# Kernel optimization log

Measured on AMD Instinct MI355X. Metric: run time of the kernel, lower is better.

Reference implementation:

```python
import jax, jax.numpy as jnp
import numpy as np

B, D, NH, HH, WW = 16, 384, 12, 48, 48
MLP = 4 * D


def _dwconv(x_blc, w, b, H, W):
    # depthwise 3x3 conv on (B,L,C) token map laid out as HxW
    Bsz, L, C = x_blc.shape
    xn = x_blc.reshape(Bsz, H, W, C).transpose(0, 3, 1, 2)  # NCHW
    y = jax.lax.conv_general_dilated(
        xn, w, (1, 1), 'SAME', feature_group_count=C,
        dimension_numbers=('NCHW', 'OIHW', 'NCHW'))
    y = y + b[None, :, None, None]
    return y.transpose(0, 2, 3, 1).reshape(Bsz, L, C)


def _ln(x, w, b):
    m = jnp.mean(x, -1, keepdims=True)
    v = jnp.mean(jnp.square(x - m), -1, keepdims=True)
    return (x - m) * jax.lax.rsqrt(v + 1e-5) * w + b


def _rope_tables(H, W, C):
    k_max = C // 4  # feature_dim // (2 * len((h, w)))
    theta = 1.0 / (10000.0 ** (jnp.arange(k_max, dtype=jnp.float32) / k_max))
    ah = jnp.broadcast_to((jnp.arange(H, dtype=jnp.float32)[:, None] * theta)[:, None, :], (H, W, k_max))
    aw = jnp.broadcast_to((jnp.arange(W, dtype=jnp.float32)[:, None] * theta)[None, :, :], (H, W, k_max))
    ang = jnp.concatenate([ah, aw], -1)  # (H, W, C//2)
    return jnp.cos(ang), jnp.sin(ang)


def _rope(x, cos, sin):
    # x: (B,H,W,C); complex rotation on consecutive pairs of the last dim
    xr = x.reshape(*x.shape[:-1], -1, 2)
    a, b2 = xr[..., 0], xr[..., 1]
    out = jnp.stack([cos * a - sin * b2, sin * a + cos * b2], -1)
    return out.reshape(x.shape)


def _forward(x, H, W, cpe1_w, cpe1_b, norm1_w, norm1_b, in_proj_w, in_proj_b,
             act_proj_w, act_proj_b, dwc_w, dwc_b, qk_w, qk_b, lepe_w, lepe_b,
             out_proj_w, out_proj_b, cpe2_w, cpe2_b, norm2_w, norm2_b,
             fc1_w, fc1_b, fc2_w, fc2_b):
    Bsz, L, C = x.shape
    nh = NH
    hd = C // nh

    x = x + _dwconv(x, cpe1_w, cpe1_b, H, W)
    shortcut = x
    xn = _ln(x, norm1_w, norm1_b)
    act_res = jax.nn.silu(xn @ act_proj_w.T + act_proj_b)
    xi = xn @ in_proj_w.T + in_proj_b
    xi = jax.nn.silu(_dwconv(xi, dwc_w, dwc_b, H, W))

    # --- linear (kernelized) attention with RoPE ---
    qk = xi @ qk_w.T + qk_b  # (B, L, 2C)
    q = jax.nn.elu(qk[..., :C]) + 1.0
    k = jax.nn.elu(qk[..., C:]) + 1.0
    cos, sin = _rope_tables(H, W, C)
    q_rope = _rope(q.reshape(Bsz, H, W, C), cos, sin).reshape(Bsz, L, nh, hd).transpose(0, 2, 1, 3)
    k_rope = _rope(k.reshape(Bsz, H, W, C), cos, sin).reshape(Bsz, L, nh, hd).transpose(0, 2, 1, 3)
    qh = q.reshape(Bsz, L, nh, hd).transpose(0, 2, 1, 3)
    kh = k.reshape(Bsz, L, nh, hd).transpose(0, 2, 1, 3)
    vh = xi.reshape(Bsz, L, nh, hd).transpose(0, 2, 1, 3)

    z = 1.0 / (jnp.einsum('bhnd,bhd->bhn', qh, kh.mean(axis=2)) + 1e-6)  # (B,nh,L)
    kv = jnp.einsum('bhnd,bhne->bhde', k_rope, vh) / L                   # (B,nh,hd,hd)
    att = jnp.einsum('bhnd,bhde->bhne', q_rope, kv) * z[..., None]
    att = att.transpose(0, 2, 1, 3).reshape(Bsz, L, C)
    att = att + _dwconv(xi, lepe_w, lepe_b, H, W)  # lepe on v (== xi)

    out = (att * act_res) @ out_proj_w.T + out_proj_b
    x = shortcut + out
    x = x + _dwconv(x, cpe2_w, cpe2_b, H, W)
    xn2 = _ln(x, norm2_w, norm2_b)
    h1 = jax.nn.gelu(xn2 @ fc1_w.T + fc1_b, approximate=False)
    x = x + (h1 @ fc2_w.T + fc2_b)
    return x


def setup_inputs() -> dict:
    key = jax.random.key(0)
    ks = jax.random.split(key, 16)
    def w(k, shape, s=0.02):
        return jax.random.normal(k, shape, jnp.float32) * s
    return {
        'x': jax.random.normal(ks[0], (B, HH * WW, D), jnp.float32),
        'H': HH, 'W': WW,
        'cpe1_w': w(ks[1], (D, 1, 3, 3)), 'cpe1_b': jnp.zeros((D,), jnp.float32),
        'norm1_w': jnp.ones((D,), jnp.float32), 'norm1_b': jnp.zeros((D,), jnp.float32),
        'in_proj_w': w(ks[2], (D, D)), 'in_proj_b': jnp.zeros((D,), jnp.float32),
        'act_proj_w': w(ks[3], (D, D)), 'act_proj_b': jnp.zeros((D,), jnp.float32),
        'dwc_w': w(ks[4], (D, 1, 3, 3)), 'dwc_b': jnp.zeros((D,), jnp.float32),
        'qk_w': w(ks[5], (2 * D, D)), 'qk_b': jnp.zeros((2 * D,), jnp.float32),
        'lepe_w': w(ks[6], (D, 1, 3, 3)), 'lepe_b': jnp.zeros((D,), jnp.float32),
        'out_proj_w': w(ks[7], (D, D)), 'out_proj_b': jnp.zeros((D,), jnp.float32),
        'cpe2_w': w(ks[8], (D, 1, 3, 3)), 'cpe2_b': jnp.zeros((D,), jnp.float32),
        'norm2_w': jnp.ones((D,), jnp.float32), 'norm2_b': jnp.zeros((D,), jnp.float32),
        'fc1_w': w(ks[9], (MLP, D)), 'fc1_b': jnp.zeros((MLP,), jnp.float32),
        'fc2_w': w(ks[10], (D, MLP)), 'fc2_b': jnp.zeros((D,), jnp.float32),
    }


def reference(x, H, W, cpe1_w, cpe1_b, norm1_w, norm1_b, in_proj_w, in_proj_b,
              act_proj_w, act_proj_b, dwc_w, dwc_b, qk_w, qk_b, lepe_w, lepe_b,
              out_proj_w, out_proj_b, cpe2_w, cpe2_b, norm2_w, norm2_b,
              fc1_w, fc1_b, fc2_w, fc2_b):
    return _forward(x, H, W, cpe1_w, cpe1_b, norm1_w, norm1_b, in_proj_w, in_proj_b,
                    act_proj_w, act_proj_b, dwc_w, dwc_b, qk_w, qk_b, lepe_w, lepe_b,
                    out_proj_w, out_proj_b, cpe2_w, cpe2_b, norm2_w, norm2_b,
                    fc1_w, fc1_b, fc2_w, fc2_b)
```

## Files before the change

kernel.cpp:

```cpp
#include <hip/hip_runtime.h>
#include <hip/hip_bf16.h>
#include <math.h>


#define L_TOK 2304
#define DIM   384
#define NHEADS 12
#define BATCH 16
#define HIMG  48
#define WIMG  48
#define UNITB ((size_t)L_TOK * DIM)

typedef unsigned short u16;
typedef __attribute__((ext_vector_type(8))) short bf16x8;
typedef __attribute__((ext_vector_type(8))) unsigned short u16x8;
typedef __attribute__((ext_vector_type(4))) float f32x4;

enum { M_BIAS = 0, M_SILU = 1, M_ELU1 = 2, M_GELU = 3, M_RES = 4 };

__device__ __forceinline__ float frcp(float x) { return __builtin_amdgcn_rcpf(x); }
__device__ __forceinline__ float siluf(float x) { return x * frcp(1.0f + __expf(-x)); }
__device__ __forceinline__ float geluf(float x) {
    float t = x * fmaf(x * x, 0.0713548162726f, 1.59576912161f);
    return x * frcp(1.0f + __expf(-t));
}
__device__ __forceinline__ u16 f2bf(float f) {
    union { __hip_bfloat16 h; u16 u; } c;
    c.h = __float2bfloat16(f);
    return c.u;
}
__device__ __forceinline__ float bf2f(u16 u) { return __uint_as_float(((unsigned)u) << 16); }
__device__ __forceinline__ float4 bf2f4(ushort4 v) {
    return (float4){bf2f(v.x), bf2f(v.y), bf2f(v.z), bf2f(v.w)};
}
__device__ __forceinline__ void vmwait(int n) {
    if (n == 0)       asm volatile("s_waitcnt vmcnt(0)" ::: "memory");
    else if (n == 4)  asm volatile("s_waitcnt vmcnt(4)" ::: "memory");
    else if (n == 8)  asm volatile("s_waitcnt vmcnt(8)" ::: "memory");
    else if (n == 12) asm volatile("s_waitcnt vmcnt(12)" ::: "memory");
    else              asm volatile("s_waitcnt vmcnt(0)" ::: "memory");
}

__global__ void sentinel_k(float* out, float v) { out[0] = v; }

__global__ __launch_bounds__(256) void cvtw_k(const float* __restrict__ src, u16* __restrict__ dst) {
    int i = blockIdx.x * 256 + threadIdx.x;
    float4 v = ((const float4*)src)[i];
    ushort4 o;
    o.x = f2bf(v.x); o.y = f2bf(v.y); o.z = f2bf(v.z); o.w = f2bf(v.w);
    ((ushort4*)dst)[i] = o;
}

__global__ __launch_bounds__(256) void rope_tab_k(float* __restrict__ cosT, float* __restrict__ sinT) {
    int i = blockIdx.x * 256 + threadIdx.x;
    if (i >= L_TOK * 192) return;
    int n = i / 192, p = i % 192;
    int h = n / WIMG, w = n % WIMG;
    int j = (p < 96) ? p : p - 96;
    float pos = (p < 96) ? (float)h : (float)w;
    float theta = expf(-(float)j * (9.210340371976184f / 96.0f));
    float ang = pos * theta;
    cosT[i] = cosf(ang);
    sinT[i] = sinf(ang);
}

#define FMA4(s, a, ww) { s.x = fmaf(a.x, ww.x, s.x); s.y = fmaf(a.y, ww.y, s.y); \
                         s.z = fmaf(a.z, ww.z, s.z); s.w = fmaf(a.w, ww.w, s.w); }

__device__ __forceinline__ void dw_remap(int& vbx, int& vby) {
    const int nstr = gridDim.y;
    vbx = blockIdx.x; vby = blockIdx.y;
    if ((nstr & 7) == 0 || (nstr & 7) == 4) {
        if ((nstr & 7) == 0) {
            const int lin = blockIdx.x + blockIdx.y * gridDim.x;
            const int x = lin & 7, k = lin >> 3;
            vby = x * (nstr >> 3) + k / gridDim.x;
            vbx = k - (k / gridDim.x) * gridDim.x;
        }
    }
}

__global__ __launch_bounds__(256) void dwconvf_k(const float* __restrict__ src,
                                                 const float* __restrict__ wgt,
                                                 const float* __restrict__ bias,
                                                 float* __restrict__ outf) {
    int vbx, vby;
    dw_remap(vbx, vby);
    const int col = vbx * 256 + threadIdx.x;
    const int strip = vby & 3;
    const int b = vby >> 2;
    const int cg = col % 96, w = col / 96;
    const int rs = WIMG * DIM;
    const size_t ibase = (size_t)b * UNITB + (size_t)w * DIM + cg * 4;
    const float* srcb = src + ibase;
    const float4 z4 = {0.f, 0.f, 0.f, 0.f};
    float4 w9[9];
#pragma unroll
    for (int t = 0; t < 9; ++t) {
        const int c = cg * 4;
        w9[t] = (float4){wgt[(c + 0) * 9 + t], wgt[(c + 1) * 9 + t],
                         wgt[(c + 2) * 9 + t], wgt[(c + 3) * 9 + t]};
    }
    const float4 bv = ((const float4*)bias)[cg];
    float4 A0, A1, A2, B0, B1, B2, C0, C1, C2;
    auto ldrow = [&](int hh, float4& L0, float4& L1, float4& L2) {
        if ((unsigned)hh >= (unsigned)HIMG) { L0 = z4; L1 = z4; L2 = z4; return; }
        const float* p = srcb + (size_t)hh * rs;
        L0 = (w > 0)        ? *(const float4*)(p - DIM) : z4;
        L1 = *(const float4*)p;
        L2 = (w < WIMG - 1) ? *(const float4*)(p + DIM) : z4;
    };
    const int h0 = strip * 12;
    ldrow(h0 - 1, A0, A1, A2);
    ldrow(h0,     B0, B1, B2);
    for (int h = h0; h < h0 + 12; ++h) {
        ldrow(h + 1, C0, C1, C2);
        float4 s = bv;
        FMA4(s, A0, w9[0]); FMA4(s, A1, w9[1]); FMA4(s, A2, w9[2]);
        FMA4(s, B0, w9[3]); FMA4(s, B1, w9[4]); FMA4(s, B2, w9[5]);
        FMA4(s, C0, w9[6]); FMA4(s, C1, w9[7]); FMA4(s, C2, w9[8]);
        const size_t idx = ibase + (size_t)h * rs;
        s.x += B1.x; s.y += B1.y; s.z += B1.z; s.w += B1.w;
        *(float4*)(outf + idx) = s;
        A0 = B0; A1 = B1; A2 = B2;
        B0 = C0; B1 = C1; B2 = C2;
    }
}

__global__ __launch_bounds__(256) void dwconvb_k(const u16* __restrict__ src,
                                                 const float* __restrict__ wgt,
                                                 const float* __restrict__ bias,
                                                 const u16* __restrict__ att,
                                                 const u16* __restrict__ act,
                                                 u16* __restrict__ outb, int mode) {
    int vbx, vby;
    dw_remap(vbx, vby);
    const int col = vbx * 256 + threadIdx.x;
    const int strip = vby & 3;
    const int b = vby >> 2;
    const int cg = col % 96, w = col / 96;
    const int rs = WIMG * DIM;
    const size_t ibase = (size_t)b * UNITB + (size_t)w * DIM + cg * 4;
    const u16* srcb = src + ibase;
    const float4 z4 = {0.f, 0.f, 0.f, 0.f};
    float4 w9[9];
#pragma unroll
    for (int t = 0; t < 9; ++t) {
        const int c = cg * 4;
        w9[t] = (float4){wgt[(c + 0) * 9 + t], wgt[(c + 1) * 9 + t],
                         wgt[(c + 2) * 9 + t], wgt[(c + 3) * 9 + t]};
    }
    const float4 bv = ((const float4*)bias)[cg];
    float4 A0, A1, A2, B0, B1, B2, C0, C1, C2;
    auto ldrow = [&](int hh, float4& L0, float4& L1, float4& L2) {
        if ((unsigned)hh >= (unsigned)HIMG) { L0 = z4; L1 = z4; L2 = z4; return; }
        const u16* p = srcb + (size_t)hh * rs;
        L0 = (w > 0)        ? bf2f4(*(const ushort4*)(p - DIM)) : z4;
        L1 = bf2f4(*(const ushort4*)p);
        L2 = (w < WIMG - 1) ? bf2f4(*(const ushort4*)(p + DIM)) : z4;
    };
    const int h0 = strip * 12;
    ldrow(h0 - 1, A0, A1, A2);
    ldrow(h0,     B0, B1, B2);
    for (int h = h0; h < h0 + 12; ++h) {
        ldrow(h + 1, C0, C1, C2);
        float4 s = bv;
        FMA4(s, A0, w9[0]); FMA4(s, A1, w9[1]); FMA4(s, A2, w9[2]);
        FMA4(s, B0, w9[3]); FMA4(s, B1, w9[4]); FMA4(s, B2, w9[5]);
        FMA4(s, C0, w9[6]); FMA4(s, C1, w9[7]); FMA4(s, C2, w9[8]);
        const size_t idx = ibase + (size_t)h * rs;
        ushort4 ob;
        if (mode == 1) {
            ob = (ushort4){f2bf(siluf(s.x)), f2bf(siluf(s.y)), f2bf(siluf(s.z)), f2bf(siluf(s.w))};
        } else {
            float4 a4 = bf2f4(*(const ushort4*)(att + idx));
            float4 m4 = bf2f4(*(const ushort4*)(act + idx));
            ob = (ushort4){f2bf((a4.x + s.x) * m4.x), f2bf((a4.y + s.y) * m4.y),
                           f2bf((a4.z + s.z) * m4.z), f2bf((a4.w + s.w) * m4.w)};
        }
        *(ushort4*)(outb + idx) = ob;
        A0 = B0; A1 = B1; A2 = B2;
        B0 = C0; B1 = C1; B2 = C2;
    }
}

__global__ __launch_bounds__(256) void ln_k(const float* __restrict__ in,
                                            const float* __restrict__ w,
                                            const float* __restrict__ b,
                                            u16* __restrict__ out) {
    const int dd = blockIdx.x;
    const int vb = (dd & 7) * (gridDim.x >> 3) + (dd >> 3);
    const int row = vb * 4 + (threadIdx.x >> 6);
    const int lane = threadIdx.x & 63;
    const float* x = in + (size_t)row * DIM;
    float v[6];
    float s = 0.f;
#pragma unroll
    for (int i = 0; i < 6; ++i) { v[i] = x[lane + i * 64]; s += v[i]; }
#pragma unroll
    for (int o = 32; o > 0; o >>= 1) s += __shfl_xor(s, o, 64);
    const float mean = s * (1.0f / DIM);
    float q = 0.f;
#pragma unroll
    for (int i = 0; i < 6; ++i) { float d = v[i] - mean; q = fmaf(d, d, q); }
#pragma unroll
    for (int o = 32; o > 0; o >>= 1) q += __shfl_xor(q, o, 64);
    const float rs = 1.0f / sqrtf(q * (1.0f / DIM) + 1e-5f);
    u16* o2 = out + (size_t)row * DIM;
#pragma unroll
    for (int i = 0; i < 6; ++i) {
        int d = lane + i * 64;
        o2[d] = f2bf(fmaf((v[i] - mean) * rs, w[d], b[d]));
    }
}

#define CHK 64
template<int K>
__global__ __launch_bounds__(256, 4) void gemm_sk(const u16* __restrict__ A, int lda,
                                                  const u16* __restrict__ Wt, int ldw,
                                                  const float* __restrict__ bias,
                                                  const float* __restrict__ bias2,
                                                  const float* __restrict__ res,
                                                  float* __restrict__ Cf, u16* __restrict__ Cb,
                                                  u16* __restrict__ Cb2,
                                                  int ldc, int mode, int mode2) {
    constexpr int NT = K / 32;
    constexpr int NCH = K / CHK;
    __shared__ u16 smem[16384];
    u16* const Bbuf[2] = {smem, smem + 8192};
    const int tid = threadIdx.x;
    const int l = tid & 63;
    const int w = tid >> 6;
    const int fr = l & 15, kb = l >> 4;
    const int T = gridDim.x * gridDim.y;
    const int d = blockIdx.y * gridDim.x + blockIdx.x;
    int flat = d;
    if ((T & 7) == 0) { const int q8 = T >> 3; flat = (d & 7) * q8 + (d >> 3); }
    const int n0 = (flat % gridDim.x) * 128;
    const int m0 = (flat / gridDim.x) * 128;
    const int sw = (fr & 7) << 4;

    f32x4 acc[2][8];
#pragma unroll
    for (int i = 0; i < 2; ++i)
#pragma unroll
        for (int j = 0; j < 8; ++j) acc[i][j] = (f32x4){0.f, 0.f, 0.f, 0.f};

    const u16* Ar0 = A + (size_t)(m0 + w * 32 + fr) * lda + kb * 8;
    const u16* Ar1 = Ar0 + (size_t)16 * lda;

    auto STAGE = [&](u16* buf, int cc) {
        const int ck0 = cc * CHK;
#pragma unroll
        for (int q = 0; q < 4; ++q) {
            const int c16 = q * 256 + tid;
            const int col = c16 >> 3;
            const int kb16 = c16 & 7;
            const int koff = ((kb16 * 16) ^ ((col & 7) << 4)) >> 1;
            const u16* g = Wt + (size_t)(n0 + col) * ldw + ck0 + koff;
            __builtin_amdgcn_global_load_lds(
                (const __attribute__((address_space(1))) void*)g,
                (__attribute__((address_space(3))) void*)(buf + (size_t)(q * 256 + w * 64) * 8),
                16, 0, 0);
        }
    };

    bf16x8 pA[4][2];
    STAGE(Bbuf[0], 0);
    __builtin_amdgcn_sched_barrier(0);
#pragma unroll
    for (int i = 0; i < 4; ++i) {
        pA[i][0] = *(const bf16x8*)(Ar0 + i * 32);
        pA[i][1] = *(const bf16x8*)(Ar1 + i * 32);
    }
    __builtin_amdgcn_sched_barrier(0);
    STAGE(Bbuf[1], 1);
    __builtin_amdgcn_sched_barrier(0);
    vmwait(12);
    __builtin_amdgcn_s_barrier();

#pragma unroll
    for (int c = 0; c < NCH; ++c) {
        const u16* bp = Bbuf[c & 1];
#pragma unroll
        for (int ks = 0; ks < 2; ++ks) {
            const int t = 2 * c + ks;
            bf16x8 a0 = pA[t & 3][0], a1 = pA[t & 3][1];
            if (t + 4 < NT) {
                pA[t & 3][0] = *(const bf16x8*)(Ar0 + (t + 4) * 32);
                pA[t & 3][1] = *(const bf16x8*)(Ar1 + (t + 4) * 32);
            }
            const int kpart = (ks * 64 + kb * 16) ^ sw;
            const char* bsb = (const char*)bp + fr * 128 + kpart;
#pragma unroll
            for (int ni = 0; ni < 8; ++ni) {
                bf16x8 bfrag = *(const bf16x8*)(bsb + ni * (16 * 128));
                acc[0][ni] = __builtin_amdgcn_mfma_f32_16x16x32_bf16(a0, bfrag, acc[0][ni], 0, 0, 0);
                acc[1][ni] = __builtin_amdgcn_mfma_f32_16x16x32_bf16(a1, bfrag, acc[1][ni], 0, 0, 0);
            }
        }
        __builtin_amdgcn_sched_barrier(0);
        __builtin_amdgcn_s_barrier();
        __builtin_amdgcn_sched_barrier(0);
        if (c + 2 < NCH) STAGE(Bbuf[c & 1], c + 2);
        __builtin_amdgcn_sched_barrier(0);
        if (c + 1 < NCH)
            vmwait((c < NCH - 2) ? 8 : 0);
    }

    const int orow = (l >> 4) * 4, ocol = l & 15;
    if (Cb != nullptr) {
        const bool is2 = (Cb2 != nullptr) && (n0 >= DIM);
        u16* dst = is2 ? Cb2 : Cb;
        const int ldcs = is2 ? DIM : ldc;
        const int nc0 = is2 ? (n0 - DIM) : n0;
        const float* bp2 = is2 ? bias2 : bias;
        const int md = is2 ? mode2 : mode;
#pragma unroll
        for (int mi = 0; mi < 2; ++mi)
#pragma unroll
            for (int ni = 0; ni < 8; ++ni) {
                const int colL = ni * 16 + ocol;
                const float bv = bp2[nc0 + colL];
#pragma unroll
                for (int r = 0; r < 4; ++r) {
                    const int rowL = w * 32 + mi * 16 + orow + r;
                    float v = acc[mi][ni][r] + bv;
                    if (md == M_SILU)      v = siluf(v);
                    else if (md == M_ELU1) v = (v > 0.f) ? (v + 1.f) : __expf(v);
                    else if (md == M_GELU) v = geluf(v);
                    smem[rowL * 128 + (colL ^ ((rowL & 7) << 3))] = f2bf(v);
                }
            }
        __builtin_amdgcn_s_barrier();
        const int rr = tid >> 4, cc = tid & 15;
#pragma unroll
        for (int it = 0; it < 8; ++it) {
            const int row = it * 16 + rr;
            u16x8 v = *(const u16x8*)&smem[row * 128 + ((cc * 8) ^ ((row & 7) << 3))];
            *(u16x8*)(dst + (size_t)(m0 + row) * ldcs + nc0 + cc * 8) = v;
        }
    } else {
        float* smf = (float*)smem;
#pragma unroll
        for (int p = 0; p < 2; ++p) {
            if (p) __builtin_amdgcn_s_barrier();
#pragma unroll
            for (int mi = 0; mi < 2; ++mi)
#pragma unroll
                for (int ni = 0; ni < 4; ++ni) {
                    const int colL = ni * 16 + ocol;
                    const float bv = bias[n0 + p * 64 + colL];
#pragma unroll
                    for (int r = 0; r < 4; ++r) {
                        const int rowL = w * 32 + mi * 16 + orow + r;
                        float v = acc[mi][p * 4 + ni][r] + bv;
                        if (mode == M_SILU)      v = siluf(v);
                        else if (mode == M_ELU1) v = (v > 0.f) ? (v + 1.f) : __expf(v);
                        else if (mode == M_GELU) v = geluf(v);
                        smf[rowL * 64 + (colL ^ ((rowL & 3) << 4))] = v;
                    }
                }
            __builtin_amdgcn_s_barrier();
            const int rr = tid >> 4, cc = tid & 15;
#pragma unroll
            for (int it = 0; it < 8; ++it) {
                const int row = it * 16 + rr;
                float4 v = *(const float4*)&smf[row * 64 + ((cc * 4) ^ ((row & 3) << 4))];
                const size_t oi = (size_t)(m0 + row) * ldc + n0 + p * 64 + cc * 4;
                if (res) {
                    float4 rv = *(const float4*)(res + oi);
                    v.x += rv.x; v.y += rv.y; v.z += rv.z; v.w += rv.w;
                }
                *(float4*)(Cf + oi) = v;
            }
        }
    }
}

__global__ __launch_bounds__(384) void kmean_part_k(const u16* __restrict__ kbuf, float* __restrict__ part, int nb) {
    const int b = blockIdx.x, chunk = blockIdx.y;
    const int c = threadIdx.x;
    const u16* p = kbuf + ((size_t)(b * L_TOK + chunk * 256)) * DIM + c;
    float s = 0.f;
    for (int n = 0; n < 256; ++n) s += bf2f(p[(size_t)n * DIM]);
    part[(size_t)(chunk * nb + b) * DIM + c] = s;
}

__global__ __launch_bounds__(384) void kmean_fin_k(const float* __restrict__ part, float* __restrict__ km, int nb) {
    const int b = blockIdx.x, c = threadIdx.x;
    float s = 0.f;
#pragma unroll
    for (int ch = 0; ch < 9; ++ch) s += part[(size_t)(ch * nb + b) * DIM + c];
    km[b * DIM + c] = s * (1.0f / L_TOK);
}

__global__ __launch_bounds__(256) void z_k(const u16* __restrict__ q, const float* __restrict__ km,
                                           float* __restrict__ z) {
    const int dd = blockIdx.x;
    const int vb = (dd & 7) * (gridDim.x >> 3) + (dd >> 3);
    const int row = vb * 4 + (threadIdx.x >> 6);
    const int lane = threadIdx.x & 63;
    const int b = row / L_TOK;
    const u16* qr = q + (size_t)row * DIM;
    const float* kb = km + b * DIM;
    float s = 0.f;
#pragma unroll
    for (int i = 0; i < 6; ++i) { int c = lane + i * 64; s += bf2f(qr[c]) * kb[c]; }
#pragma unroll
    for (int o = 32; o > 0; o >>= 1) s += __shfl_xor(s, o, 64);
    if (lane == 0) z[row] = 1.0f / (s + 1e-6f);
}

__global__ __launch_bounds__(256) void kv_part_k(const u16* __restrict__ kbuf, const u16* __restrict__ xi,
                                                 const float* __restrict__ cosT, const float* __restrict__ sinT,
                                                 float* __restrict__ part) {
    const int bh = blockIdx.x >> 2, chunk = blockIdx.x & 3;
    const int b = bh / NHEADS, h = bh % NHEADS;
    __shared__ float ks[64][33];
    __shared__ float vs[64][33];
    const int tid = threadIdx.x;
    const int e0 = (tid & 15) * 2;
    const int d0 = (tid >> 4) * 2;
    float acc00 = 0.f, acc01 = 0.f, acc10 = 0.f, acc11 = 0.f;
    const int nbeg = chunk * 576, nend = nbeg + 576;
    for (int n0 = nbeg; n0 < nend; n0 += 64) {
#pragma unroll
        for (int j = 0; j < 4; ++j) {
            int pi = tid + j * 256;
            int tn = pi >> 4;
            int pd = pi & 15;
            int n = n0 + tn;
            unsigned kk = *(const unsigned*)(kbuf + ((size_t)(b * L_TOK + n)) * DIM + h * 32 + pd * 2);
            float ka = bf2f((u16)(kk & 0xffffu)), kb2 = bf2f((u16)(kk >> 16));
            float cs = cosT[n * 192 + h * 16 + pd];
            float sn = sinT[n * 192 + h * 16 + pd];
            ks[tn][pd * 2]     = cs * ka - sn * kb2;
            ks[tn][pd * 2 + 1] = sn * ka + cs * kb2;
        }
#pragma unroll
        for (int j = 0; j < 4; ++j) {
            int pi = tid + j * 256;
            int tn = pi >> 4;
            int dd = (pi & 15) * 2;
            unsigned vv = *(const unsigned*)(xi + ((size_t)(b * L_TOK + n0 + tn)) * DIM + h * 32 + dd);
            vs[tn][dd]     = bf2f((u16)(vv & 0xffffu));
            vs[tn][dd + 1] = bf2f((u16)(vv >> 16));
        }
        __syncthreads();
#pragma unroll 8
        for (int n = 0; n < 64; ++n) {
            float k0v = ks[n][d0], k1v = ks[n][d0 + 1];
            float v0 = vs[n][e0], v1 = vs[n][e0 + 1];
            acc00 = fmaf(k0v, v0, acc00);
            acc01 = fmaf(k0v, v1, acc01);
            acc10 = fmaf(k1v, v0, acc10);
            acc11 = fmaf(k1v, v1, acc11);
        }
        __syncthreads();
    }
    float* o = part + ((size_t)blockIdx.x * 32 + d0) * 32 + e0;
    o[0] = acc00; o[1] = acc01;
    o[32] = acc10; o[33] = acc11;
}

__global__ __launch_bounds__(256) void kv_fin_k(const float* __restrict__ part, u16* __restrict__ kvt) {
    const int bh = blockIdx.x;
    const int tid = threadIdx.x;
#pragma unroll
    for (int i = tid; i < 1024; i += 256) {
        const int e = i >> 5, dd = i & 31;
        float s = 0.f;
#pragma unroll
        for (int c = 0; c < 4; ++c) s += part[((size_t)(bh * 4 + c)) * 1024 + dd * 32 + e];
        kvt[(size_t)bh * 1024 + i] = f2bf(s * (1.0f / L_TOK));
    }
}

__global__ __launch_bounds__(256) void attm_k(const u16* __restrict__ q, const u16* __restrict__ kvt,
                                              const float* __restrict__ z,
                                              const float* __restrict__ cosT, const float* __restrict__ sinT,
                                              u16* __restrict__ out) {
    __shared__ u16 ost[128 * 32];
    const int tid = threadIdx.x, l = tid & 63, w = tid >> 6;
    const int b = blockIdx.y / NHEADS, h = blockIdx.y % NHEADS;
    const int m0 = blockIdx.x * 128;
    const int fr = l & 15, kb = l >> 4;

    f32x4 acc[2][2];
#pragma unroll
    for (int i = 0; i < 2; ++i)
#pragma unroll
        for (int j = 0; j < 2; ++j) acc[i][j] = (f32x4){0.f, 0.f, 0.f, 0.f};

    const int p0 = h * 16 + kb * 4;
    bf16x8 afr[2];
#pragma unroll
    for (int mi = 0; mi < 2; ++mi) {
        const int n = m0 + w * 32 + mi * 16 + fr;
        bf16x8 raw = *(const bf16x8*)(q + ((size_t)(b * L_TOK + n)) * DIM + h * 32 + kb * 8);
        float4 cs = *(const float4*)(cosT + (size_t)n * 192 + p0);
        float4 sn = *(const float4*)(sinT + (size_t)n * 192 + p0);
        union { u16 u[8]; bf16x8 v; } pk;
        float a0, a1;
        a0 = bf2f((u16)raw[0]); a1 = bf2f((u16)raw[1]);
        pk.u[0] = f2bf(cs.x * a0 - sn.x * a1); pk.u[1] = f2bf(sn.x * a0 + cs.x * a1);
        a0 = bf2f((u16)raw[2]); a1 = bf2f((u16)raw[3]);
        pk.u[2] = f2bf(cs.y * a0 - sn.y * a1); pk.u[3] = f2bf(sn.y * a0 + cs.y * a1);
        a0 = bf2f((u16)raw[4]); a1 = bf2f((u16)raw[5]);
        pk.u[4] = f2bf(cs.z * a0 - sn.z * a1); pk.u[5] = f2bf(sn.z * a0 + cs.z * a1);
        a0 = bf2f((u16)raw[6]); a1 = bf2f((u16)raw[7]);
        pk.u[6] = f2bf(cs.w * a0 - sn.w * a1); pk.u[7] = f2bf(sn.w * a0 + cs.w * a1);
        afr[mi] = pk.v;
    }
    bf16x8 bfr[2];
    const u16* kvh = kvt + (size_t)(b * NHEADS + h) * 1024;
#pragma unroll
    for (int ni = 0; ni < 2; ++ni)
        bfr[ni] = *(const bf16x8*)(kvh + (ni * 16 + fr) * 32 + kb * 8);
#pragma unroll
    for (int mi = 0; mi < 2; ++mi)
#pragma unroll
        for (int ni = 0; ni < 2; ++ni)
            acc[mi][ni] = __builtin_amdgcn_mfma_f32_16x16x32_bf16(afr[mi], bfr[ni], acc[mi][ni], 0, 0, 0);

    const int orow = (l >> 4) * 4, ocol = l & 15;
#pragma unroll
    for (int mi = 0; mi < 2; ++mi) {
        float zz[4];
#pragma unroll
        for (int r = 0; r < 4; ++r)
            zz[r] = z[b * L_TOK + m0 + w * 32 + mi * 16 + orow + r];
#pragma unroll
        for (int ni = 0; ni < 2; ++ni) {
#pragma unroll
            for (int r = 0; r < 4; ++r) {
                const int rowL = w * 32 + mi * 16 + orow + r;
                ost[rowL * 32 + ni * 16 + ocol] = f2bf(acc[mi][ni][r] * zz[r]);
            }
        }
    }
    __syncthreads();
#pragma unroll
    for (int it = 0; it < 2; ++it) {
        const int ch = it * 256 + tid;
        const int row = ch >> 2, c8 = (ch & 3) * 8;
        u16x8 v = *(const u16x8*)&ost[row * 32 + c8];
        *(u16x8*)(out + ((size_t)(b * L_TOK + m0 + row)) * DIM + h * 32 + c8) = v;
    }
}

extern "C" void kernel_launch(void* const* d_in, const int* in_sizes, int n_in,
                              void* d_out, int out_size, void* d_ws, size_t ws_size,
                              hipStream_t stream) {
    const float* x       = (const float*)d_in[0];
    const float* cpe1_w  = (const float*)d_in[3];
    const float* cpe1_b  = (const float*)d_in[4];
    const float* norm1_w = (const float*)d_in[5];
    const float* norm1_b = (const float*)d_in[6];
    const float* in_w    = (const float*)d_in[7];
    const float* in_b    = (const float*)d_in[8];
    const float* act_w   = (const float*)d_in[9];
    const float* act_b   = (const float*)d_in[10];
    const float* dwc_w   = (const float*)d_in[11];
    const float* dwc_b   = (const float*)d_in[12];
    const float* qk_w    = (const float*)d_in[13];
    const float* qk_b    = (const float*)d_in[14];
    const float* lepe_w  = (const float*)d_in[15];
    const float* lepe_b  = (const float*)d_in[16];
    const float* outp_w  = (const float*)d_in[17];
    const float* outp_b  = (const float*)d_in[18];
    const float* cpe2_w  = (const float*)d_in[19];
    const float* cpe2_b  = (const float*)d_in[20];
    const float* norm2_w = (const float*)d_in[21];
    const float* norm2_b = (const float*)d_in[22];
    const float* fc1_w   = (const float*)d_in[23];
    const float* fc1_b   = (const float*)d_in[24];
    const float* fc2_w   = (const float*)d_in[25];
    const float* fc2_b   = (const float*)d_in[26];
    float* out = (float*)d_out;

    float* ws = (float*)d_ws;
    const size_t TAB = (size_t)L_TOK * 192;
    const size_t NW_IN = 147456, NW_QK = 294912, NW_FC = 589824;
    const size_t WBF_U16 = NW_IN * 3 + NW_QK + NW_FC * 2;
    const size_t KVP = 4 * (size_t)BATCH * NHEADS * 1024;
    const size_t ZB  = (size_t)BATCH * L_TOK;
    const size_t SMALL = 2 * TAB + (size_t)BATCH * DIM + 9 * (size_t)BATCH * DIM
                       + (size_t)BATCH * NHEADS * 1024 + KVP + ZB + WBF_U16 / 2;
    float* cosT = ws;
    float* sinT = cosT + TAB;
    float* km   = sinT + TAB;
    float* part = km + (size_t)BATCH * DIM;
    float* kvb  = part + 9 * (size_t)BATCH * DIM;
    float* kvp  = kvb + (size_t)BATCH * NHEADS * 1024;
    float* zb   = kvp + KVP;
    u16*   kvt  = (u16*)kvb;
    u16*   wb_in  = (u16*)(zb + ZB);
    u16*   wb_act = wb_in + NW_IN;
    u16*   wb_qk  = wb_act + NW_IN;
    u16*   wb_out = wb_qk + NW_QK;
    u16*   wb_fc1 = wb_out + NW_IN;
    u16*   wb_fc2 = wb_fc1 + NW_FC;
    float* gbuf = ws + SMALL;

    const size_t avail = (ws_size / 4 > SMALL) ? (ws_size / 4 - SMALL) : 0;
    int nb = 0;
    for (int cand = BATCH; cand >= 1; cand >>= 1)
        if (9 * (size_t)cand * UNITB / 2 <= avail) { nb = cand; break; }
    if (nb == 0) {
        sentinel_k<<<1, 1, 0, stream>>>(out, (float)(ws_size >> 20));
        return;
    }

    cvtw_k<<<(int)(NW_IN / 1024), 256, 0, stream>>>(in_w, wb_in);
    cvtw_k<<<(int)(NW_IN / 1024), 256, 0, stream>>>(act_w, wb_act);
    cvtw_k<<<(int)(NW_QK / 1024), 256, 0, stream>>>(qk_w, wb_qk);
    cvtw_k<<<(int)(NW_IN / 1024), 256, 0, stream>>>(outp_w, wb_out);
    cvtw_k<<<(int)(NW_FC / 1024), 256, 0, stream>>>(fc1_w, wb_fc1);
    cvtw_k<<<(int)(NW_FC / 1024), 256, 0, stream>>>(fc2_w, wb_fc2);
    rope_tab_k<<<(int)((TAB + 255) / 256), 256, 0, stream>>>(cosT, sinT);

    for (int b0 = 0; b0 < BATCH; b0 += nb) {
        const size_t goff = (size_t)b0 * UNITB;
        const size_t GU   = (size_t)nb * UNITB;
        float* W0 = gbuf;
        float* W1 = gbuf + GU;
        float* W2 = gbuf + 2 * GU;
        u16*   Wb = (u16*)(gbuf + 4 * GU);
        float* O  = out + goff;
        const float* Xg = x + goff;
        u16* xi0p = (u16*)W2;
        u16* actp = (u16*)W2 + GU;

        const dim3 DWG(18, nb * 4);
        const dim3 G384(3, nb * 18), G768(6, nb * 18), G1536(12, nb * 18);

        dwconvf_k<<<DWG, 256, 0, stream>>>(Xg, cpe1_w, cpe1_b, W0);
        ln_k<<<nb * 576, 256, 0, stream>>>(W0, norm1_w, norm1_b, (u16*)W1);
        gemm_sk<384><<<G768, 256, 0, stream>>>((u16*)W1, DIM, wb_in, DIM, in_b, act_b, nullptr,
                                               nullptr, xi0p, actp, DIM, M_BIAS, M_SILU);
        dwconvb_k<<<DWG, 256, 0, stream>>>(xi0p, dwc_w, dwc_b, nullptr, nullptr, Wb, 1);
        gemm_sk<384><<<G768, 256, 0, stream>>>(Wb, DIM, wb_qk, DIM, qk_b, qk_b + DIM, nullptr,
                                               nullptr, (u16*)W1, (u16*)O, DIM, M_ELU1, M_ELU1);
        kmean_part_k<<<dim3(nb, 9), 384, 0, stream>>>((u16*)O, part, nb);
        kmean_fin_k<<<nb, 384, 0, stream>>>(part, km, nb);
        z_k<<<nb * 576, 256, 0, stream>>>((u16*)W1, km, zb);
        kv_part_k<<<nb * NHEADS * 4, 256, 0, stream>>>((u16*)O, Wb, cosT, sinT, kvp);
        kv_fin_k<<<nb * NHEADS, 256, 0, stream>>>(kvp, kvt);
        attm_k<<<dim3(18, nb * NHEADS), 256, 0, stream>>>((u16*)W1, kvt, zb, cosT, sinT, (u16*)O);
        dwconvb_k<<<DWG, 256, 0, stream>>>(Wb, lepe_w, lepe_b, (const u16*)O, actp,
                                           (u16*)W1, 3);
        gemm_sk<384><<<G384, 256, 0, stream>>>((u16*)W1, DIM, wb_out, DIM, outp_b, nullptr, W0,
                                               W2, nullptr, nullptr, DIM, M_RES, M_RES);
        dwconvf_k<<<DWG, 256, 0, stream>>>(W2, cpe2_w, cpe2_b, W0);
        ln_k<<<nb * 576, 256, 0, stream>>>(W0, norm2_w, norm2_b, (u16*)W1);
        gemm_sk<384><<<G1536, 256, 0, stream>>>((u16*)W1, DIM, wb_fc1, DIM, fc1_b, nullptr, nullptr,
                                                nullptr, (u16*)W2, nullptr, 1536, M_GELU, M_GELU);
        gemm_sk<1536><<<G384, 256, 0, stream>>>((u16*)W2, 1536, wb_fc2, 1536, fc2_b, nullptr, W0,
                                                O, nullptr, nullptr, DIM, M_RES, M_RES);
    }
}
```

Baseline: 510.5 us.

## Fuse depthwise CPE conv with LayerNorm into a single kernel

Replaces the separate fp32 depthwise-conv kernel and LayerNorm kernel with one kernel, dwln_k. Each 384-thread block handles 4 tokens, computes the 3x3 conv plus residual directly from neighbours, writes the fp32 result, and then reduces mean and variance through shared memory to emit the normalized bf16 output. This removes one launch and the re-read of the fp32 conv output by the LN pass. In exchange, the row-streaming register reuse of conv inputs is lost, so neighbouring rows are re-read from cache. Variance is now computed as E[x^2]-mean^2, which is less numerically robust.

```diff
diff --git a/kernel.cpp b/kernel.cpp
--- a/kernel.cpp
+++ b/kernel.cpp
@@ -67,33 +67,23 @@
 #define FMA4(s, a, ww) { s.x = fmaf(a.x, ww.x, s.x); s.y = fmaf(a.y, ww.y, s.y); \
                          s.z = fmaf(a.z, ww.z, s.z); s.w = fmaf(a.w, ww.w, s.w); }
 
-__device__ __forceinline__ void dw_remap(int& vbx, int& vby) {
-    const int nstr = gridDim.y;
-    vbx = blockIdx.x; vby = blockIdx.y;
-    if ((nstr & 7) == 0 || (nstr & 7) == 4) {
-        if ((nstr & 7) == 0) {
-            const int lin = blockIdx.x + blockIdx.y * gridDim.x;
-            const int x = lin & 7, k = lin >> 3;
-            vby = x * (nstr >> 3) + k / gridDim.x;
-            vbx = k - (k / gridDim.x) * gridDim.x;
-        }
-    }
-}
-
-__global__ __launch_bounds__(256) void dwconvf_k(const float* __restrict__ src,
-                                                 const float* __restrict__ wgt,
-                                                 const float* __restrict__ bias,
-                                                 float* __restrict__ outf) {
-    int vbx, vby;
-    dw_remap(vbx, vby);
-    const int col = vbx * 256 + threadIdx.x;
-    const int strip = vby & 3;
-    const int b = vby >> 2;
-    const int cg = col % 96, w = col / 96;
-    const int rs = WIMG * DIM;
-    const size_t ibase = (size_t)b * UNITB + (size_t)w * DIM + cg * 4;
-    const float* srcb = src + ibase;
-    const float4 z4 = {0.f, 0.f, 0.f, 0.f};
+__global__ __launch_bounds__(384) void dwln_k(const float* __restrict__ src,
+                                              const float* __restrict__ wgt,
+                                              const float* __restrict__ bias,
+                                              const float* __restrict__ nw,
+                                              const float* __restrict__ nb_,
+                                              float* __restrict__ outf,
+                                              u16* __restrict__ outn) {
+    const int T = 12 * gridDim.y;
+    int lin = blockIdx.x + blockIdx.y * 12;
+    { const int x = lin & 7, k = lin >> 3; lin = x * (T >> 3) + k; }
+    const int vbx = lin % 12, vby = lin / 12;
+    const int tok = threadIdx.x / 96, cg = threadIdx.x % 96;
+    const int w = vbx * 4 + tok;
+    const int h = vby % HIMG;
+    const int b = vby / HIMG;
+    const size_t base = (size_t)b * UNITB + cg * 4;
+
     float4 w9[9];
 #pragma unroll
     for (int t = 0; t < 9; ++t) {
@@ -101,29 +91,62 @@
         w9[t] = (float4){wgt[(c + 0) * 9 + t], wgt[(c + 1) * 9 + t],
                          wgt[(c + 2) * 9 + t], wgt[(c + 3) * 9 + t]};
     }
-    const float4 bv = ((const float4*)bias)[cg];
-    float4 A0, A1, A2, B0, B1, B2, C0, C1, C2;
-    auto ldrow = [&](int hh, float4& L0, float4& L1, float4& L2) {
-        if ((unsigned)hh >= (unsigned)HIMG) { L0 = z4; L1 = z4; L2 = z4; return; }
-        const float* p = srcb + (size_t)hh * rs;
-        L0 = (w > 0)        ? *(const float4*)(p - DIM) : z4;
-        L1 = *(const float4*)p;
-        L2 = (w < WIMG - 1) ? *(const float4*)(p + DIM) : z4;
-    };
-    const int h0 = strip * 12;
-    ldrow(h0 - 1, A0, A1, A2);
-    ldrow(h0,     B0, B1, B2);
-    for (int h = h0; h < h0 + 12; ++h) {
-        ldrow(h + 1, C0, C1, C2);
-        float4 s = bv;
-        FMA4(s, A0, w9[0]); FMA4(s, A1, w9[1]); FMA4(s, A2, w9[2]);
-        FMA4(s, B0, w9[3]); FMA4(s, B1, w9[4]); FMA4(s, B2, w9[5]);
-        FMA4(s, C0, w9[6]); FMA4(s, C1, w9[7]); FMA4(s, C2, w9[8]);
-        const size_t idx = ibase + (size_t)h * rs;
-        s.x += B1.x; s.y += B1.y; s.z += B1.z; s.w += B1.w;
-        *(float4*)(outf + idx) = s;
-        A0 = B0; A1 = B1; A2 = B2;
-        B0 = C0; B1 = C1; B2 = C2;
+    float4 s = ((const float4*)bias)[cg];
+    float4 ctr = {0.f, 0.f, 0.f, 0.f};
+#pragma unroll
+    for (int dh = 0; dh < 3; ++dh) {
+        const int hh = h + dh - 1;
+        if ((unsigned)hh >= (unsigned)HIMG) continue;
+#pragma unroll
+        for (int dw = 0; dw < 3; ++dw) {
+            const int ww = w + dw - 1;
+            if ((unsigned)ww >= (unsigned)WIMG) continue;
+            float4 v = *(const float4*)(src + base + (size_t)(hh * WIMG + ww) * DIM);
+            if (dh == 1 && dw == 1) ctr = v;
+            FMA4(s, v, w9[dh * 3 + dw]);
+        }
+    }
+    s.x += ctr.x; s.y += ctr.y; s.z += ctr.z; s.w += ctr.w;
+    const size_t oidx = base + (size_t)(h * WIMG + w) * DIM;
+    *(float4*)(outf + oidx) = s;
+
+    __shared__ float rS[384], rQ[384];
+    __shared__ float mv[8];
+    rS[threadIdx.x] = s.x + s.y + s.z + s.w;
+    rQ[threadIdx.x] = s.x * s.x + s.y * s.y + s.z * s.z + s.w * s.w;
+    __syncthreads();
+    if (cg < 32) {
+        float a  = rS[threadIdx.x] + rS[threadIdx.x + 32] + rS[threadIdx.x + 64];
+        float qq = rQ[threadIdx.x] + rQ[threadIdx.x + 32] + rQ[threadIdx.x + 64];
+#pragma unroll
+        for (int o = 16; o > 0; o >>= 1) { a += __shfl_xor(a, o); qq += __shfl_xor(qq, o); }
+        if (cg == 0) {
+            const float mean = a * (1.0f / DIM);
+            const float var = qq * (1.0f / DIM) - mean * mean;
+            mv[tok * 2]     = mean;
+            mv[tok * 2 + 1] = 1.0f / sqrtf(var + 1e-5f);
+        }
+    }
+    __syncthreads();
+    const float mean = mv[tok * 2], rstd = mv[tok * 2 + 1];
+    const float4 nwv = ((const float4*)nw)[cg];
+    const float4 nbv = ((const float4*)nb_)[cg];
+    ushort4 o;
+    o.x = f2bf(fmaf((s.x - mean) * rstd, nwv.x, nbv.x));
+    o.y = f2bf(fmaf((s.y - mean) * rstd, nwv.y, nbv.y));
+    o.z = f2bf(fmaf((s.z - mean) * rstd, nwv.z, nbv.z));
+    o.w = f2bf(fmaf((s.w - mean) * rstd, nwv.w, nbv.w));
+    *(ushort4*)(outn + oidx) = o;
+}
+
+__device__ __forceinline__ void dw_remap(int& vbx, int& vby) {
+    const int nstr = gridDim.y;
+    vbx = blockIdx.x; vby = blockIdx.y;
+    if ((nstr & 7) == 0) {
+        const int lin = blockIdx.x + blockIdx.y * gridDim.x;
+        const int x = lin & 7, k = lin >> 3;
+        vby = x * (nstr >> 3) + k / gridDim.x;
+        vbx = k - (k / gridDim.x) * gridDim.x;
     }
 }
 
@@ -181,36 +204,6 @@
         *(ushort4*)(outb + idx) = ob;
         A0 = B0; A1 = B1; A2 = B2;
         B0 = C0; B1 = C1; B2 = C2;
-    }
-}
-
-__global__ __launch_bounds__(256) void ln_k(const float* __restrict__ in,
-                                            const float* __restrict__ w,
-                                            const float* __restrict__ b,
-                                            u16* __restrict__ out) {
-    const int dd = blockIdx.x;
-    const int vb = (dd & 7) * (gridDim.x >> 3) + (dd >> 3);
-    const int row = vb * 4 + (threadIdx.x >> 6);
-    const int lane = threadIdx.x & 63;
-    const float* x = in + (size_t)row * DIM;
-    float v[6];
-    float s = 0.f;
-#pragma unroll
-    for (int i = 0; i < 6; ++i) { v[i] = x[lane + i * 64]; s += v[i]; }
-#pragma unroll
-    for (int o = 32; o > 0; o >>= 1) s += __shfl_xor(s, o, 64);
-    const float mean = s * (1.0f / DIM);
-    float q = 0.f;
-#pragma unroll
-    for (int i = 0; i < 6; ++i) { float d = v[i] - mean; q = fmaf(d, d, q); }
-#pragma unroll
-    for (int o = 32; o > 0; o >>= 1) q += __shfl_xor(q, o, 64);
-    const float rs = 1.0f / sqrtf(q * (1.0f / DIM) + 1e-5f);
-    u16* o2 = out + (size_t)row * DIM;
-#pragma unroll
-    for (int i = 0; i < 6; ++i) {
-        int d = lane + i * 64;
-        o2[d] = f2bf(fmaf((v[i] - mean) * rs, w[d], b[d]));
     }
 }
 
@@ -634,10 +627,10 @@
         u16* actp = (u16*)W2 + GU;
 
         const dim3 DWG(18, nb * 4);
+        const dim3 DLG(12, nb * 48);
         const dim3 G384(3, nb * 18), G768(6, nb * 18), G1536(12, nb * 18);
 
-        dwconvf_k<<<DWG, 256, 0, stream>>>(Xg, cpe1_w, cpe1_b, W0);
-        ln_k<<<nb * 576, 256, 0, stream>>>(W0, norm1_w, norm1_b, (u16*)W1);
+        dwln_k<<<DLG, 384, 0, stream>>>(Xg, cpe1_w, cpe1_b, norm1_w, norm1_b, W0, (u16*)W1);
         gemm_sk<384><<<G768, 256, 0, stream>>>((u16*)W1, DIM, wb_in, DIM, in_b, act_b, nullptr,
                                                nullptr, xi0p, actp, DIM, M_BIAS, M_SILU);
         dwconvb_k<<<DWG, 256, 0, stream>>>(xi0p, dwc_w, dwc_b, nullptr, nullptr, Wb, 1);
@@ -653,8 +646,7 @@
                                            (u16*)W1, 3);
         gemm_sk<384><<<G384, 256, 0, stream>>>((u16*)W1, DIM, wb_out, DIM, outp_b, nullptr, W0,
                                                W2, nullptr, nullptr, DIM, M_RES, M_RES);
-        dwconvf_k<<<DWG, 256, 0, stream>>>(W2, cpe2_w, cpe2_b, W0);
-        ln_k<<<nb * 576, 256, 0, stream>>>(W0, norm2_w, norm2_b, (u16*)W1);
+        dwln_k<<<DLG, 384, 0, stream>>>(W2, cpe2_w, cpe2_b, norm2_w, norm2_b, W0, (u16*)W1);
         gemm_sk<384><<<G1536, 256, 0, stream>>>((u16*)W1, DIM, wb_fc1, DIM, fc1_b, nullptr, nullptr,
                                                 nullptr, (u16*)W2, nullptr, 1536, M_GELU, M_GELU);
         gemm_sk<1536><<<G384, 256, 0, stream>>>((u16*)W2, 1536, wb_fc2, 1536, fc2_b, nullptr, W0,
```

New measurement: 555.1 us. +8.7%, slower.
